# Kernel tuning notes

Measured on AMD Instinct MI355X. Metric: run time of the kernel, lower is better.

The kernel has to match this reference:

```python
import jax, jax.numpy as jnp
import numpy as np

V, BS, E, H, L, FC = 50257, 1024, 768, 12, 6, 4
B, T = 4, 1024
HS = E // H
FF = FC * E
EPS = 1e-5


def setup_inputs() -> dict:
    key = jax.random.key(0)
    ks = jax.random.split(key, 24)
    s = 0.02
    inp = {
        'idx': jax.random.randint(ks[0], (B, T), 0, V),
        'targets': jax.random.randint(ks[1], (B, T), 0, V),
        'tok_emb': jax.random.normal(ks[2], (V, E), jnp.float32) * s,
        'pos_emb': jax.random.normal(ks[3], (BS, E), jnp.float32) * s,
        'Wq': jax.random.normal(ks[4], (L, H, E, HS), jnp.float32) * s,
        'Wk': jax.random.normal(ks[5], (L, H, E, HS), jnp.float32) * s,
        'Wv': jax.random.normal(ks[6], (L, H, E, HS), jnp.float32) * s,
        'Wo': jax.random.normal(ks[7], (L, E, E), jnp.float32) * s,
        'bo': jnp.zeros((L, E), jnp.float32),
        'ln1_s': jnp.ones((L, E), jnp.float32),
        'ln1_b': jnp.zeros((L, E), jnp.float32),
        'ln2_s': jnp.ones((L, E), jnp.float32),
        'ln2_b': jnp.zeros((L, E), jnp.float32),
        'W1': jax.random.normal(ks[8], (L, E, FF), jnp.float32) * s,
        'b1': jnp.zeros((L, FF), jnp.float32),
        'W2': jax.random.normal(ks[9], (L, FF, E), jnp.float32) * s,
        'b2': jnp.zeros((L, E), jnp.float32),
        'lnf_s': jnp.ones((E,), jnp.float32),
        'lnf_b': jnp.zeros((E,), jnp.float32),
        'Wlm': jax.random.normal(ks[10], (E, V), jnp.float32) * s,
        'blm': jnp.zeros((V,), jnp.float32),
    }
    return inp


def _ln(x, scale, bias):
    mu = x.mean(-1, keepdims=True)
    var = ((x - mu) ** 2).mean(-1, keepdims=True)
    return (x - mu) * jax.lax.rsqrt(var + EPS) * scale + bias


def _forward(idx, targets, tok_emb, pos_emb, Wq, Wk, Wv, Wo, bo,
             ln1_s, ln1_b, ln2_s, ln2_b, W1, b1, W2, b2,
             lnf_s, lnf_b, Wlm, blm):
    Bc, Tc = idx.shape
    x = tok_emb[idx] + pos_emb[:Tc]                      # [B,T,E]
    causal = jnp.tril(jnp.ones((Tc, Tc), bool))          # [T,T]

    def block(x, p):
        wq, wk, wv, wo_, bo_, l1s, l1b, l2s, l2b, w1, b1_, w2, b2_ = p
        h = _ln(x, l1s, l1b)
        q = jnp.einsum('bte,hed->bhtd', h, wq)
        k = jnp.einsum('bte,hed->bhtd', h, wk)
        v = jnp.einsum('bte,hed->bhtd', h, wv)
        scores = jnp.einsum('bhtd,bhsd->bhts', q, k) * (HS ** -0.5)
        scores = jnp.where(causal, scores, -jnp.inf)
        att = jax.nn.softmax(scores, axis=-1)            # [B,H,T,T]
        o = jnp.einsum('bhts,bhsd->bhtd', att, v)
        o = o.transpose(0, 2, 1, 3).reshape(Bc, Tc, E)   # concat heads
        x = x + jnp.einsum('bte,ef->btf', o, wo_) + bo_
        h2 = _ln(x, l2s, l2b)
        f = jax.nn.relu(jnp.einsum('bte,ef->btf', h2, w1) + b1_)
        x = x + jnp.einsum('btf,fe->bte', f, w2) + b2_
        return x, None

    layers = (Wq, Wk, Wv, Wo, bo, ln1_s, ln1_b, ln2_s, ln2_b, W1, b1, W2, b2)
    x, _ = jax.lax.scan(block, x, layers)
    x = _ln(x, lnf_s, lnf_b)
    logits = jnp.einsum('bte,ev->btv', x, Wlm) + blm     # [B,T,V]
    logp = jax.nn.log_softmax(logits, axis=-1)
    nll = -jnp.take_along_axis(logp, targets[..., None], axis=-1)[..., 0]
    loss = nll.mean()
    return logits, loss


def reference(idx, targets, tok_emb, pos_emb, Wq, Wk, Wv, Wo, bo,
              ln1_s, ln1_b, ln2_s, ln2_b, W1, b1, W2, b2,
              lnf_s, lnf_b, Wlm, blm):
    return _forward(idx, targets, tok_emb, pos_emb, Wq, Wk, Wv, Wo, bo,
                    ln1_s, ln1_b, ln2_s, ln2_b, W1, b1, W2, b2,
                    lnf_s, lnf_b, Wlm, blm)
```

## Files before the change

### kernel.cpp

```cpp
#include <hip/hip_runtime.h>
#include <hip/hip_bf16.h>
#include <cstdint>
#include <cstddef>

#define NB 4
#define NT 1024
#define NE 768
#define NH 12
#define NHS 64
#define NL 6
#define NFF 3072
#define NV 50257
#define NVP 50304
#define NTOK (NB*NT)
#define NCB_LM (NVP/128)
#define QKVS 2304

typedef __attribute__((ext_vector_type(8))) short short8;
typedef __attribute__((ext_vector_type(4))) float f32x4;
typedef __hip_bfloat16 bf16;

__global__ __launch_bounds__(256) void embed_kernel(
    const int* __restrict__ idx, const float* __restrict__ tok,
    const float* __restrict__ pos, float* __restrict__ x)
{
  int bt = blockIdx.x;
  int token = idx[bt];
  int t = bt & (NT - 1);
  const float* tr = tok + (size_t)token * NE;
  const float* pr = pos + (size_t)t * NE;
  float* xr = x + (size_t)bt * NE;
  for (int i = threadIdx.x; i < NE; i += 256)
    xr[i] = tr[i] + pr[i];
}

__global__ __launch_bounds__(256) void ln_kernel(
    const float* __restrict__ in, const float* __restrict__ sc,
    const float* __restrict__ bi, bf16* __restrict__ out)
{
  int row = blockIdx.x, tid = threadIdx.x;
  const float* xr = in + (size_t)row * NE;
  float v0 = xr[tid], v1 = xr[tid + 256], v2 = xr[tid + 512];
  float s = v0 + v1 + v2;
  float ss = v0 * v0 + v1 * v1 + v2 * v2;
  #pragma unroll
  for (int o = 32; o > 0; o >>= 1) {
    s  += __shfl_xor(s, o);
    ss += __shfl_xor(ss, o);
  }
  __shared__ float r1[4], r2[4];
  if ((tid & 63) == 0) { r1[tid >> 6] = s; r2[tid >> 6] = ss; }
  __syncthreads();
  float tot = r1[0] + r1[1] + r1[2] + r1[3];
  float tss = r2[0] + r2[1] + r2[2] + r2[3];
  float mu  = tot * (1.f / NE);
  float var = tss * (1.f / NE) - mu * mu;
  float rs  = rsqrtf(var + 1e-5f);
  bf16* orow = out + (size_t)row * NE;
  orow[tid]       = __float2bfloat16((v0 - mu) * rs * sc[tid]       + bi[tid]);
  orow[tid + 256] = __float2bfloat16((v1 - mu) * rs * sc[tid + 256] + bi[tid + 256]);
  orow[tid + 512] = __float2bfloat16((v2 - mu) * rs * sc[tid + 512] + bi[tid + 512]);
}

__global__ __launch_bounds__(256) void tconv_kernel(
    const float* __restrict__ src, bf16* __restrict__ dst,
    int R, int Cs, int Cd, int zdiv,
    size_t srcZstr, size_t dstLstr, size_t dstHstr)
{
  __shared__ float t[32][33];
  int z = blockIdx.z;
  int l = z / zdiv, h = z - l * zdiv;
  src += (size_t)z * srcZstr;
  dst += (size_t)l * dstLstr + (size_t)h * dstHstr;
  int c0 = blockIdx.x * 32, r0 = blockIdx.y * 32;
  int tx = threadIdx.x & 31, ty = threadIdx.x >> 5;
  #pragma unroll
  for (int i = 0; i < 32; i += 8) {
    int r = r0 + ty + i, c = c0 + tx;
    t[ty + i][tx] = (c < Cs) ? src[(size_t)r * Cs + c] : 0.f;
  }
  __syncthreads();
  #pragma unroll
  for (int i = 0; i < 32; i += 8) {
    int c = c0 + ty + i, r = r0 + tx;
    if (c < Cd) dst[(size_t)c * R + r] = __float2bfloat16(t[tx][ty + i]);
  }
}

template<int MREP, bool SWZ>
__global__ __launch_bounds__(256) void gemm_bf(
    const bf16* __restrict__ A,
    const bf16* __restrict__ BT,
    float* __restrict__ Cf, bf16* __restrict__ Cbf,
    const float* __restrict__ bias, const float* __restrict__ Rres,
    float* __restrict__ ps,
    int M, int N, int K, int relu, int ncb)
{
  constexpr int BMT = MREP * 32;
  __shared__ bf16 As[BMT][64];
  __shared__ bf16 Bs[128][64];
  __shared__ float ps2[BMT][2];
  int tid = threadIdx.x;
  int lane = tid & 63;
  int w = __builtin_amdgcn_readfirstlane(tid >> 6);
  int wr = w >> 1, wc = w & 1;
  int cb = blockIdx.x;
  int row0 = blockIdx.y * BMT;
  int col0 = cb * 128;

  f32x4 acc[MREP][4] = {};

  for (int k0 = 0; k0 < K; k0 += 64) {
    #pragma unroll
    for (int r = 0; r < MREP; ++r) {
      int c = r * 256 + tid;
      int trow = c >> 3;
      int schunk = SWZ ? ((c & 7) ^ (trow & 7)) : (c & 7);
      const bf16* ga = A + (size_t)(row0 + trow) * K + k0 + (schunk << 3);
      __builtin_amdgcn_global_load_lds(
          (const __attribute__((address_space(1))) void*)ga,
          (__attribute__((address_space(3))) void*)((char*)&As[0][0] + (unsigned)c * 16),
          16, 0, 0);
    }
    #pragma unroll
    for (int r = 0; r < 4; ++r) {
      int c = r * 256 + tid;
      int trow = c >> 3;
      int schunk = SWZ ? ((c & 7) ^ (trow & 7)) : (c & 7);
      const bf16* gb = BT + (size_t)(col0 + trow) * K + k0 + (schunk << 3);
      __builtin_amdgcn_global_load_lds(
          (const __attribute__((address_space(1))) void*)gb,
          (__attribute__((address_space(3))) void*)((char*)&Bs[0][0] + (unsigned)c * 16),
          16, 0, 0);
    }
    __syncthreads();
    int l15 = lane & 15;
    int g8 = (lane >> 4) << 3;
    int sx = SWZ ? ((l15 & 7) << 3) : 0;
    #pragma unroll
    for (int kk = 0; kk < 64; kk += 32) {
      short8 a[MREP], b[4];
      #pragma unroll
      for (int m = 0; m < MREP; ++m)
        a[m] = *(const short8*)&As[wr * (MREP * 16) + m * 16 + l15][(kk + g8) ^ sx];
      #pragma unroll
      for (int n = 0; n < 4; ++n)
        b[n] = *(const short8*)&Bs[wc * 64 + n * 16 + l15][(kk + g8) ^ sx];
      #pragma unroll
      for (int m = 0; m < MREP; ++m)
        #pragma unroll
        for (int n = 0; n < 4; ++n)
          acc[m][n] = __builtin_amdgcn_mfma_f32_16x16x32_bf16(a[m], b[n], acc[m][n], 0, 0, 0);
    }
    __syncthreads();
  }

  int cr = lane >> 4;
  int cc = lane & 15;
  #pragma unroll
  for (int m = 0; m < MREP; ++m) {
    #pragma unroll
    for (int n = 0; n < 4; ++n) {
      int col = col0 + wc * 64 + n * 16 + cc;
      if (col >= N) continue;
      float bv = bias ? bias[col] : 0.f;
      #pragma unroll
      for (int e = 0; e < 4; ++e) {
        int row = row0 + wr * (MREP * 16) + m * 16 + cr * 4 + e;
        float v = acc[m][n][e] + bv;
        size_t off = (size_t)row * N + col;
        if (Rres) v += Rres[off];
        if (relu) v = fmaxf(v, 0.f);
        if (Cf)  Cf[off] = v;
        if (Cbf) Cbf[off] = __float2bfloat16(v);
      }
    }
  }

  if (ps) {
    #pragma unroll
    for (int m = 0; m < MREP; ++m) {
      #pragma unroll
      for (int e = 0; e < 4; ++e) {
        float ssum = 0.f;
        #pragma unroll
        for (int n = 0; n < 4; ++n) {
          int col = col0 + wc * 64 + n * 16 + cc;
          float val = (col < N) ? (acc[m][n][e] + (bias ? bias[col] : 0.f)) : -1e30f;
          ssum += __expf(val);
        }
        ssum += __shfl_xor(ssum, 1);
        ssum += __shfl_xor(ssum, 2);
        ssum += __shfl_xor(ssum, 4);
        ssum += __shfl_xor(ssum, 8);
        if (cc == 0) {
          int rl = wr * (MREP * 16) + m * 16 + cr * 4 + e;
          ps2[rl][wc] = ssum;
        }
      }
    }
    __syncthreads();
    for (int i = tid; i < BMT; i += 256) {
      size_t o = (size_t)(row0 + i) * ncb + cb;
      ps[o] = ps2[i][0] + ps2[i][1];
    }
  }
}

static __device__ inline unsigned short bfbits(float x) {
  bf16 h = __float2bfloat16(x);
  return *reinterpret_cast<unsigned short*>(&h);
}

__global__ __launch_bounds__(256) void fattn_kernel(
    const bf16* __restrict__ QKV, bf16* __restrict__ O)
{
  __shared__ unsigned short Ks[64][72];
  __shared__ unsigned short Vt[64][72];
  __shared__ unsigned short Pl[4][16][72];
  int qt = blockIdx.x, h = blockIdx.y, b = blockIdx.z;
  int tid = threadIdx.x;
  int lane = tid & 63;
  int w = tid >> 6;
  int l15 = lane & 15, g = lane >> 4;
  int brow = b * NT;
  int qbase = qt * 64;
  int q_loc = w * 16 + l15;

  short8 bq[2];
  {
    const bf16* qp = QKV + (size_t)(brow + qbase + q_loc) * QKVS + h * 64 + g * 8;
    bq[0] = *(const short8*)qp;
    bq[1] = *(const short8*)(qp + 32);
  }

  float m_run = -1e30f, l_run = 0.f;
  f32x4 acc[4] = {};

  for (int kt = 0; kt <= qt; ++kt) {
    int s0 = kt * 64;
    #pragma unroll
    for (int i = 0; i < 2; ++i) {
      int c = tid + i * 256;
      int row = c >> 3, colg = (c & 7) * 8;
      const bf16* kp = QKV + (size_t)(brow + s0 + row) * QKVS + NE + h * 64 + colg;
      const bf16* vp = QKV + (size_t)(brow + s0 + row) * QKVS + 2 * NE + h * 64 + colg;
      short8 kv = *(const short8*)kp;
      short8 vv = *(const short8*)vp;
      *(short8*)&Ks[row][colg] = kv;
      #pragma unroll
      for (int j = 0; j < 8; ++j)
        Vt[colg + j][row] = (unsigned short)vv[j];
    }
    __syncthreads();

    f32x4 sf[4] = {};
    #pragma unroll
    for (int kk = 0; kk < 2; ++kk) {
      #pragma unroll
      for (int m = 0; m < 4; ++m) {
        short8 a = *(const short8*)&Ks[m * 16 + l15][kk * 32 + g * 8];
        sf[m] = __builtin_amdgcn_mfma_f32_16x16x32_bf16(a, bq[kk], sf[m], 0, 0, 0);
      }
    }

    float sv[4][4];
    float mx = -1e30f;
    bool diag = (kt == qt);
    #pragma unroll
    for (int m = 0; m < 4; ++m)
      #pragma unroll
      for (int e = 0; e < 4; ++e) {
        float v = sf[m][e] * 0.125f;
        if (diag) {
          int sl = m * 16 + g * 4 + e;
          if (sl > q_loc) v = -1e30f;
        }
        sv[m][e] = v;
        mx = fmaxf(mx, v);
      }
    mx = fmaxf(mx, __shfl_xor(mx, 16));
    mx = fmaxf(mx, __shfl_xor(mx, 32));
    float m_new = fmaxf(m_run, mx);
    float p[4][4];
    float rs = 0.f;
    #pragma unroll
    for (int m = 0; m < 4; ++m)
      #pragma unroll
      for (int e = 0; e < 4; ++e) {
        float pe = __expf(sv[m][e] - m_new);
        p[m][e] = pe;
        rs += pe;
      }
    rs += __shfl_xor(rs, 16);
    rs += __shfl_xor(rs, 32);
    float sc_old = __expf(m_run - m_new);
    l_run = l_run * sc_old + rs;
    m_run = m_new;
    #pragma unroll
    for (int dm = 0; dm < 4; ++dm)
      #pragma unroll
      for (int e = 0; e < 4; ++e)
        acc[dm][e] *= sc_old;

    #pragma unroll
    for (int m = 0; m < 4; ++m)
      #pragma unroll
      for (int ep = 0; ep < 2; ++ep) {
        unsigned u = (unsigned)bfbits(p[m][2 * ep]) |
                     ((unsigned)bfbits(p[m][2 * ep + 1]) << 16);
        *(unsigned*)&Pl[w][l15][m * 16 + g * 4 + ep * 2] = u;
      }

    #pragma unroll
    for (int ks = 0; ks < 2; ++ks) {
      short8 pb = *(const short8*)&Pl[w][l15][ks * 32 + g * 8];
      #pragma unroll
      for (int dm = 0; dm < 4; ++dm) {
        short8 av = *(const short8*)&Vt[dm * 16 + l15][ks * 32 + g * 8];
        acc[dm] = __builtin_amdgcn_mfma_f32_16x16x32_bf16(av, pb, acc[dm], 0, 0, 0);
      }
    }
    __syncthreads();
  }

  float inv = 1.f / l_run;
  bf16* op = O + (size_t)(brow + qbase + q_loc) * NE + h * 64;
  #pragma unroll
  for (int dm = 0; dm < 4; ++dm)
    #pragma unroll
    for (int ep = 0; ep < 2; ++ep) {
      int d = dm * 16 + g * 4 + ep * 2;
      unsigned u = (unsigned)bfbits(acc[dm][2 * ep] * inv) |
                   ((unsigned)bfbits(acc[dm][2 * ep + 1] * inv) << 16);
      *(unsigned*)((unsigned short*)op + d) = u;
    }
}

__global__ __launch_bounds__(128) void nll_finish(
    const float* __restrict__ ps,
    const float* __restrict__ logits, const int* __restrict__ targets,
    float* __restrict__ nll)
{
  int row = blockIdx.x, tid = threadIdx.x;
  float s = 0.f;
  for (int i = tid; i < NCB_LM; i += 128)
    s += ps[(size_t)row * NCB_LM + i];
  #pragma unroll
  for (int o = 32; o > 0; o >>= 1) s += __shfl_xor(s, o);
  __shared__ float ss[2];
  if ((tid & 63) == 0) ss[tid >> 6] = s;
  __syncthreads();
  if (tid == 0) {
    float S = ss[0] + ss[1];
    float tgt = logits[(size_t)row * NV + targets[row]];
    nll[row] = logf(S) - tgt;
  }
}

__global__ __launch_bounds__(256) void loss_kernel(
    const float* __restrict__ nll, float* __restrict__ out)
{
  int tid = threadIdx.x;
  float s = 0.f;
  for (int i = tid; i < NTOK; i += 256) s += nll[i];
  #pragma unroll
  for (int o = 32; o > 0; o >>= 1) s += __shfl_xor(s, o);
  __shared__ float red[4];
  if ((tid & 63) == 0) red[tid >> 6] = s;
  __syncthreads();
  if (tid == 0) out[0] = (red[0] + red[1] + red[2] + red[3]) * (1.f / NTOK);
}

static inline void gemm(const bf16* A, const bf16* BT,
                        float* Cf, bf16* Cbf,
                        const float* bias, const float* Rres, float* ps,
                        int M, int N, int Npad, int K, int relu,
                        int mrep, hipStream_t st)
{
  int ncb = Npad / 128;
  dim3 g(ncb, M / (mrep * 32));
  if (mrep == 4)
    gemm_bf<4, true><<<g, dim3(256), 0, st>>>(A, BT, Cf, Cbf, bias, Rres, ps, M, N, K, relu, ncb);
  else
    gemm_bf<2, true><<<g, dim3(256), 0, st>>>(A, BT, Cf, Cbf, bias, Rres, ps, M, N, K, relu, ncb);
}

extern "C" void kernel_launch(void* const* d_in, const int* in_sizes, int n_in,
                              void* d_out, int out_size, void* d_ws, size_t ws_size,
                              hipStream_t stream)
{
  const int*   idx     = (const int*)  d_in[0];
  const int*   targets = (const int*)  d_in[1];
  const float* tok_emb = (const float*)d_in[2];
  const float* pos_emb = (const float*)d_in[3];
  const float* Wq      = (const float*)d_in[4];
  const float* Wk      = (const float*)d_in[5];
  const float* Wv      = (const float*)d_in[6];
  const float* Wo      = (const float*)d_in[7];
  const float* bo      = (const float*)d_in[8];
  const float* ln1_s   = (const float*)d_in[9];
  const float* ln1_b   = (const float*)d_in[10];
  const float* ln2_s   = (const float*)d_in[11];
  const float* ln2_b   = (const float*)d_in[12];
  const float* W1      = (const float*)d_in[13];
  const float* b1      = (const float*)d_in[14];
  const float* W2      = (const float*)d_in[15];
  const float* b2      = (const float*)d_in[16];
  const float* lnf_s   = (const float*)d_in[17];
  const float* lnf_b   = (const float*)d_in[18];
  const float* Wlm     = (const float*)d_in[19];
  const float* blm     = (const float*)d_in[20];
  float* out = (float*)d_out;

  const size_t XE = (size_t)NTOK * NE;
  char* p = (char*)d_ws;
  float* x     = (float*)p;         p += XE * 4;
  bf16* h_bf   = (bf16*)p;          p += XE * 2;
  bf16* qkv_bf = (bf16*)p;          p += (size_t)NTOK * QKVS * 2;
  bf16* att_bf = (bf16*)p;          p += XE * 2;
  bf16* f_bf   = (bf16*)p;          p += (size_t)NTOK * NFF * 2;
  bf16* wqkv_a = (bf16*)p;          p += (size_t)NL * QKVS * NE * 2;
  bf16* wto_a  = (bf16*)p;          p += (size_t)NL * NE * NE * 2;
  bf16* wt1_a  = (bf16*)p;          p += (size_t)NL * NFF * NE * 2;
  bf16* wt2_a  = (bf16*)p;          p += (size_t)NL * NE * NFF * 2;
  bf16* wtlm   = (bf16*)p;          p += (size_t)NVP * NE * 2;
  float* psb   = (float*)p;         p += (size_t)NTOK * NCB_LM * 4;
  float* nll   = (float*)p;         p += (size_t)NTOK * 4;

  embed_kernel<<<dim3(NTOK), dim3(256), 0, stream>>>(idx, tok_emb, pos_emb, x);

  tconv_kernel<<<dim3(2, 24, NL * NH), dim3(256), 0, stream>>>(
      Wq, wqkv_a, NE, NHS, NHS, NH,
      (size_t)NE * NHS, (size_t)QKVS * NE, (size_t)NHS * NE);
  tconv_kernel<<<dim3(2, 24, NL * NH), dim3(256), 0, stream>>>(
      Wk, wqkv_a + (size_t)NE * NE, NE, NHS, NHS, NH,
      (size_t)NE * NHS, (size_t)QKVS * NE, (size_t)NHS * NE);
  tconv_kernel<<<dim3(2, 24, NL * NH), dim3(256), 0, stream>>>(
      Wv, wqkv_a + (size_t)2 * NE * NE, NE, NHS, NHS, NH,
      (size_t)NE * NHS, (size_t)QKVS * NE, (size_t)NHS * NE);
  tconv_kernel<<<dim3(24, 24, NL), dim3(256), 0, stream>>>(
      Wo, wto_a, NE, NE, NE, 1, (size_t)NE * NE, (size_t)NE * NE, 0);
  tconv_kernel<<<dim3(96, 24, NL), dim3(256), 0, stream>>>(
      W1, wt1_a, NE, NFF, NFF, 1, (size_t)NE * NFF, (size_t)NFF * NE, 0);
  tconv_kernel<<<dim3(24, 96, NL), dim3(256), 0, stream>>>(
      W2, wt2_a, NFF, NE, NE, 1, (size_t)NFF * NE, (size_t)NE * NFF, 0);
  tconv_kernel<<<dim3(NVP / 32, 24, 1), dim3(256), 0, stream>>>(
      Wlm, wtlm, NE, NV, NVP, 1, 0, 0, 0);

  for (int l = 0; l < NL; ++l) {
    ln_kernel<<<dim3(NTOK), dim3(256), 0, stream>>>(x, ln1_s + l*NE, ln1_b + l*NE, h_bf);

    gemm(h_bf, wqkv_a + (size_t)l * QKVS * NE, nullptr, qkv_bf, nullptr, nullptr, nullptr,
         NTOK, QKVS, QKVS, NE, 0, 4, stream);

    fattn_kernel<<<dim3(NT / 64, NH, NB), dim3(256), 0, stream>>>(qkv_bf, att_bf);

    gemm(att_bf, wto_a + (size_t)l * NE * NE, x, nullptr, bo + l*NE, x, nullptr,
         NTOK, NE, NE, NE, 0, 2, stream);

    ln_kernel<<<dim3(NTOK), dim3(256), 0, stream>>>(x, ln2_s + l*NE, ln2_b + l*NE, h_bf);

    gemm(h_bf, wt1_a + (size_t)l * NFF * NE, nullptr, f_bf, b1 + l*NFF, nullptr, nullptr,
         NTOK, NFF, NFF, NE, 1, 4, stream);
    gemm(f_bf, wt2_a + (size_t)l * NE * NFF, x, nullptr, b2 + l*NE, x, nullptr,
         NTOK, NE, NE, NFF, 0, 2, stream);
  }

  ln_kernel<<<dim3(NTOK), dim3(256), 0, stream>>>(x, lnf_s, lnf_b, h_bf);

  {
    dim3 g(NCB_LM, NTOK / 128);
    gemm_bf<4, false><<<g, dim3(256), 0, stream>>>(
        h_bf, wtlm, out, nullptr, blm, nullptr, psb,
        NTOK, NV, NE, 0, NCB_LM);
  }

  nll_finish<<<dim3(NTOK), dim3(128), 0, stream>>>(psb, out, targets, nll);
  loss_kernel<<<dim3(1), dim3(256), 0, stream>>>(nll, out + (size_t)NTOK * NV);
}
```

Baseline: 2.353 ms.

## Add dedicated LM-head GEMM with direct global-to-LDS double-buffered loads

Replaces the generic gemm_bf call for the LM head with a specialized 128x128 tile kernel. It uses global_load_lds to copy A and B tiles straight into LDS, double-buffered over K steps of 32, so loads overlap the MFMA work. The kernel keeps the fused bias add and per-row exp-sum partials for the later log-softmax. The LDS tile is unpadded, so the fragment reads risk bank conflicts. The generic kernel's partial-sum write loop bound also changes from BMT to MREP*32.

```diff
diff --git a/kernel.cpp b/kernel.cpp
--- a/kernel.cpp
+++ b/kernel.cpp
@@ -200,11 +200,139 @@
       }
     }
     __syncthreads();
-    for (int i = tid; i < BMT; i += 256) {
+    for (int i = tid; i < MREP * 32; i += 256) {
       size_t o = (size_t)(row0 + i) * ncb + cb;
       ps[o] = ps2[i][0] + ps2[i][1];
     }
   }
+}
+
+#define LBK 32
+__global__ __launch_bounds__(256) void lm_gemm(
+    const bf16* __restrict__ A, const bf16* __restrict__ BT,
+    float* __restrict__ Cf, const float* __restrict__ bias,
+    float* __restrict__ ps, int M, int N, int K, int ncb)
+{
+  __shared__ bf16 As[2][128][LBK];
+  __shared__ bf16 Bs[2][128][LBK];
+  __shared__ float ps2[128][2];
+  int tid = threadIdx.x;
+  int lane = tid & 63;
+  int w = __builtin_amdgcn_readfirstlane(tid >> 6);
+  int wr = w >> 1, wc = w & 1;
+  int row0 = blockIdx.y * 128, col0 = blockIdx.x * 128;
+  int l15 = lane & 15;
+  int g8 = (lane >> 4) << 3;
+
+  f32x4 acc[4][4] = {};
+  const int nk = K / LBK;
+
+#define LM_STAGE(b, k0)                                                        \
+  {                                                                            \
+    _Pragma("unroll")                                                          \
+    for (int r = 0; r < 2; ++r) {                                              \
+      int c = r * 256 + tid;                                                   \
+      int trow = c >> 2, tcol = (c & 3) << 3;                                  \
+      const bf16* ga = A + (size_t)(row0 + trow) * K + (k0) + tcol;            \
+      __builtin_amdgcn_global_load_lds(                                        \
+          (const __attribute__((address_space(1))) void*)ga,                   \
+          (__attribute__((address_space(3))) void*)((char*)&As[b][0][0] + (unsigned)c * 16), \
+          16, 0, 0);                                                           \
+    }                                                                          \
+    _Pragma("unroll")                                                          \
+    for (int r = 0; r < 2; ++r) {                                              \
+      int c = r * 256 + tid;                                                   \
+      int trow = c >> 2, tcol = (c & 3) << 3;                                  \
+      const bf16* gb = BT + (size_t)(col0 + trow) * K + (k0) + tcol;           \
+      __builtin_amdgcn_global_load_lds(                                        \
+          (const __attribute__((address_space(1))) void*)gb,                   \
+          (__attribute__((address_space(3))) void*)((char*)&Bs[b][0][0] + (unsigned)c * 16), \
+          16, 0, 0);                                                           \
+    }                                                                          \
+  }
+
+  LM_STAGE(0, 0);
+  asm volatile("s_waitcnt vmcnt(0)" ::: "memory");
+  __builtin_amdgcn_s_barrier();
+
+  int cur = 0;
+  for (int t = 0; t < nk - 1; ++t) {
+    LM_STAGE(cur ^ 1, (t + 1) * LBK);
+    short8 a[4], bb[4];
+    #pragma unroll
+    for (int m = 0; m < 4; ++m)
+      a[m] = *(const short8*)&As[cur][wr * 64 + m * 16 + l15][g8];
+    #pragma unroll
+    for (int n = 0; n < 4; ++n)
+      bb[n] = *(const short8*)&Bs[cur][wc * 64 + n * 16 + l15][g8];
+    #pragma unroll
+    for (int m = 0; m < 4; ++m)
+      #pragma unroll
+      for (int n = 0; n < 4; ++n)
+        acc[m][n] = __builtin_amdgcn_mfma_f32_16x16x32_bf16(a[m], bb[n], acc[m][n], 0, 0, 0);
+    asm volatile("s_waitcnt vmcnt(0)" ::: "memory");
+    __builtin_amdgcn_s_barrier();
+    cur ^= 1;
+  }
+  {
+    short8 a[4], bb[4];
+    #pragma unroll
+    for (int m = 0; m < 4; ++m)
+      a[m] = *(const short8*)&As[cur][wr * 64 + m * 16 + l15][g8];
+    #pragma unroll
+    for (int n = 0; n < 4; ++n)
+      bb[n] = *(const short8*)&Bs[cur][wc * 64 + n * 16 + l15][g8];
+    #pragma unroll
+    for (int m = 0; m < 4; ++m)
+      #pragma unroll
+      for (int n = 0; n < 4; ++n)
+        acc[m][n] = __builtin_amdgcn_mfma_f32_16x16x32_bf16(a[m], bb[n], acc[m][n], 0, 0, 0);
+  }
+
+  int cr = lane >> 4;
+  int cc = lane & 15;
+  #pragma unroll
+  for (int m = 0; m < 4; ++m) {
+    #pragma unroll
+    for (int n = 0; n < 4; ++n) {
+      int col = col0 + wc * 64 + n * 16 + cc;
+      if (col >= N) continue;
+      float bv = bias[col];
+      #pragma unroll
+      for (int e = 0; e < 4; ++e) {
+        int row = row0 + wr * 64 + m * 16 + cr * 4 + e;
+        Cf[(size_t)row * N + col] = acc[m][n][e] + bv;
+      }
+    }
+  }
+
+  #pragma unroll
+  for (int m = 0; m < 4; ++m) {
+    #pragma unroll
+    for (int e = 0; e < 4; ++e) {
+      float ssum = 0.f;
+      #pragma unroll
+      for (int n = 0; n < 4; ++n) {
+        int col = col0 + wc * 64 + n * 16 + cc;
+        float val = (col < N) ? (acc[m][n][e] + bias[col]) : -1e30f;
+        ssum += __expf(val);
+      }
+      ssum += __shfl_xor(ssum, 1);
+      ssum += __shfl_xor(ssum, 2);
+      ssum += __shfl_xor(ssum, 4);
+      ssum += __shfl_xor(ssum, 8);
+      if (cc == 0) {
+        int rl = wr * 64 + m * 16 + cr * 4 + e;
+        ps2[rl][wc] = ssum;
+      }
+    }
+  }
+  __syncthreads();
+  for (int i = tid; i < 128; i += 256) {
+    size_t o = (size_t)(row0 + i) * ncb + blockIdx.x;
+    ps[o] = ps2[i][0] + ps2[i][1];
+  }
+#undef LM_STAGE
 }
 
 static __device__ inline unsigned short bfbits(float x) {
@@ -471,9 +599,8 @@
 
   {
     dim3 g(NCB_LM, NTOK / 128);
-    gemm_bf<4, false><<<g, dim3(256), 0, stream>>>(
-        h_bf, wtlm, out, nullptr, blm, nullptr, psb,
-        NTOK, NV, NE, 0, NCB_LM);
+    lm_gemm<<<g, dim3(256), 0, stream>>>(h_bf, wtlm, out, blm, psb,
+                                         NTOK, NV, NE, NCB_LM);
   }
 
   nll_finish<<<dim3(NTOK), dim3(128), 0, stream>>>(psb, out, targets, nll);
```

After: 2.170 ms. 7.8% less time.

## Multi-buffer GEMM LDS tiles with async prefetch and a K-step of 32

Applied to the files above, without the earlier changes.

Replaces the single-buffered GEMM with a multi-stage pipeline that shrinks the K-tile to 32 and keeps 2 or 3 LDS buffers. The next tile's global-to-LDS loads are issued before the current tile's MFMAs, with explicit vmcnt waits and one barrier per step instead of two. This is meant to hide global load latency behind compute, most of all in the large LM-head GEMM, which uses depth 3. In exchange, each barrier covers less work and the hand-tuned vmcnt counts depend on how many loads each stage issues, so the ordering is fragile.

```diff
diff --git a/kernel.cpp b/kernel.cpp
--- a/kernel.cpp
+++ b/kernel.cpp
@@ -87,72 +87,85 @@
   }
 }
 
-template<int MREP, bool SWZ>
-__global__ __launch_bounds__(256) void gemm_bf(
-    const bf16* __restrict__ A,
-    const bf16* __restrict__ BT,
+template<int MREP, int DEPTH, bool SWZ>
+__global__ __launch_bounds__(256) void pgemm(
+    const bf16* __restrict__ A, const bf16* __restrict__ BT,
     float* __restrict__ Cf, bf16* __restrict__ Cbf,
     const float* __restrict__ bias, const float* __restrict__ Rres,
     float* __restrict__ ps,
     int M, int N, int K, int relu, int ncb)
 {
   constexpr int BMT = MREP * 32;
-  __shared__ bf16 As[BMT][64];
-  __shared__ bf16 Bs[128][64];
+  constexpr int AIT = (MREP * 128) / 256;
+  constexpr int SWAIT = AIT + 2;
+  __shared__ bf16 As[DEPTH][BMT][32];
+  __shared__ bf16 Bs[DEPTH][128][32];
   __shared__ float ps2[BMT][2];
   int tid = threadIdx.x;
   int lane = tid & 63;
   int w = __builtin_amdgcn_readfirstlane(tid >> 6);
   int wr = w >> 1, wc = w & 1;
-  int cb = blockIdx.x;
   int row0 = blockIdx.y * BMT;
-  int col0 = cb * 128;
+  int col0 = blockIdx.x * 128;
+  int l15 = lane & 15;
+  int g8 = (lane >> 4) << 3;
+  const int nk = K / 32;
 
   f32x4 acc[MREP][4] = {};
 
-  for (int k0 = 0; k0 < K; k0 += 64) {
-    #pragma unroll
-    for (int r = 0; r < MREP; ++r) {
+  auto STAGE = [&](int b, int t) {
+    int k0 = t * 32;
+    #pragma unroll
+    for (int r = 0; r < AIT; ++r) {
       int c = r * 256 + tid;
-      int trow = c >> 3;
-      int schunk = SWZ ? ((c & 7) ^ (trow & 7)) : (c & 7);
-      const bf16* ga = A + (size_t)(row0 + trow) * K + k0 + (schunk << 3);
+      int trow = c >> 2;
+      int sch = SWZ ? ((c & 3) ^ (trow & 3)) : (c & 3);
+      const bf16* ga = A + (size_t)(row0 + trow) * K + k0 + (sch << 3);
       __builtin_amdgcn_global_load_lds(
           (const __attribute__((address_space(1))) void*)ga,
-          (__attribute__((address_space(3))) void*)((char*)&As[0][0] + (unsigned)c * 16),
+          (__attribute__((address_space(3))) void*)((char*)&As[b][0][0] + (unsigned)c * 16),
           16, 0, 0);
     }
     #pragma unroll
-    for (int r = 0; r < 4; ++r) {
+    for (int r = 0; r < 2; ++r) {
       int c = r * 256 + tid;
-      int trow = c >> 3;
-      int schunk = SWZ ? ((c & 7) ^ (trow & 7)) : (c & 7);
-      const bf16* gb = BT + (size_t)(col0 + trow) * K + k0 + (schunk << 3);
+      int trow = c >> 2;
+      int sch = SWZ ? ((c & 3) ^ (trow & 3)) : (c & 3);
+      const bf16* gb = BT + (size_t)(col0 + trow) * K + k0 + (sch << 3);
       __builtin_amdgcn_global_load_lds(
           (const __attribute__((address_space(1))) void*)gb,
-          (__attribute__((address_space(3))) void*)((char*)&Bs[0][0] + (unsigned)c * 16),
+          (__attribute__((address_space(3))) void*)((char*)&Bs[b][0][0] + (unsigned)c * 16),
           16, 0, 0);
     }
-    __syncthreads();
-    int l15 = lane & 15;
-    int g8 = (lane >> 4) << 3;
-    int sx = SWZ ? ((l15 & 7) << 3) : 0;
-    #pragma unroll
-    for (int kk = 0; kk < 64; kk += 32) {
-      short8 a[MREP], b[4];
-      #pragma unroll
-      for (int m = 0; m < MREP; ++m)
-        a[m] = *(const short8*)&As[wr * (MREP * 16) + m * 16 + l15][(kk + g8) ^ sx];
+  };
+
+  STAGE(0, 0);
+  if (DEPTH == 3 && nk > 1) STAGE(1, 1);
+
+  for (int t = 0; t < nk; ++t) {
+    if (DEPTH == 3 && t + 1 < nk) {
+      if (SWAIT == 4) asm volatile("s_waitcnt vmcnt(4)" ::: "memory");
+      else            asm volatile("s_waitcnt vmcnt(3)" ::: "memory");
+    } else {
+      asm volatile("s_waitcnt vmcnt(0)" ::: "memory");
+    }
+    __builtin_amdgcn_s_barrier();
+    if (t + DEPTH - 1 < nk) STAGE((t + DEPTH - 1) % DEPTH, t + DEPTH - 1);
+
+    int b = t % DEPTH;
+    int sx = SWZ ? ((l15 & 3) << 3) : 0;
+    short8 a[MREP], bb[4];
+    #pragma unroll
+    for (int m = 0; m < MREP; ++m)
+      a[m] = *(const short8*)&As[b][wr * (MREP * 16) + m * 16 + l15][g8 ^ sx];
+    #pragma unroll
+    for (int n = 0; n < 4; ++n)
+      bb[n] = *(const short8*)&Bs[b][wc * 64 + n * 16 + l15][g8 ^ sx];
+    #pragma unroll
+    for (int m = 0; m < MREP; ++m)
       #pragma unroll
       for (int n = 0; n < 4; ++n)
-        b[n] = *(const short8*)&Bs[wc * 64 + n * 16 + l15][(kk + g8) ^ sx];
-      #pragma unroll
-      for (int m = 0; m < MREP; ++m)
-        #pragma unroll
-        for (int n = 0; n < 4; ++n)
-          acc[m][n] = __builtin_amdgcn_mfma_f32_16x16x32_bf16(a[m], b[n], acc[m][n], 0, 0, 0);
-    }
-    __syncthreads();
+        acc[m][n] = __builtin_amdgcn_mfma_f32_16x16x32_bf16(a[m], bb[n], acc[m][n], 0, 0, 0);
   }
 
   int cr = lane >> 4;
@@ -201,7 +214,7 @@
     }
     __syncthreads();
     for (int i = tid; i < BMT; i += 256) {
-      size_t o = (size_t)(row0 + i) * ncb + cb;
+      size_t o = (size_t)(row0 + i) * ncb + blockIdx.x;
       ps[o] = ps2[i][0] + ps2[i][1];
     }
   }
@@ -381,9 +394,9 @@
   int ncb = Npad / 128;
   dim3 g(ncb, M / (mrep * 32));
   if (mrep == 4)
-    gemm_bf<4, true><<<g, dim3(256), 0, st>>>(A, BT, Cf, Cbf, bias, Rres, ps, M, N, K, relu, ncb);
+    pgemm<4, 2, true><<<g, dim3(256), 0, st>>>(A, BT, Cf, Cbf, bias, Rres, ps, M, N, K, relu, ncb);
   else
-    gemm_bf<2, true><<<g, dim3(256), 0, st>>>(A, BT, Cf, Cbf, bias, Rres, ps, M, N, K, relu, ncb);
+    pgemm<2, 2, true><<<g, dim3(256), 0, st>>>(A, BT, Cf, Cbf, bias, Rres, ps, M, N, K, relu, ncb);
 }
 
 extern "C" void kernel_launch(void* const* d_in, const int* in_sizes, int n_in,
@@ -471,7 +484,7 @@
 
   {
     dim3 g(NCB_LM, NTOK / 128);
-    gemm_bf<4, false><<<g, dim3(256), 0, stream>>>(
+    pgemm<4, 3, false><<<g, dim3(256), 0, stream>>>(
         h_bf, wtlm, out, nullptr, blm, nullptr, psb,
         NTOK, NV, NE, 0, NCB_LM);
   }
```

After: 2.344 ms. No clear change (-0.4%).
